# Performance work log

Measured on AMD Instinct MI355X. Metric: run time of the kernel, lower is better.

The kernel has to match this reference:

```python
import jax, jax.numpy as jnp
import numpy as np

B, S, N, F, H = 8, 12, 4096, 4, 64  # batch, seq_len, num_nodes, input_dim, hidden_dim


def setup_inputs() -> dict:
    key = jax.random.key(0)
    ks = jax.random.split(key, 16)
    sc = 0.05
    adj = jax.random.uniform(ks[0], (N, N), jnp.float32) * (2.0 / N)  # ~row-normalized Laplacian
    return {
        "X": jax.random.normal(ks[1], (B, S, N, F), jnp.float32),
        "adj": adj,
        "struc_emb": jax.random.normal(ks[2], (N, H), jnp.float32),
        "W1": jax.random.normal(ks[3], (H + F, 3 * H), jnp.float32) * sc,
        "b1": jnp.ones((3 * H,), jnp.float32),  # bias=1.0 init in graph_conv1
        "W2": jax.random.normal(ks[4], (H + F, H), jnp.float32) * sc,
        "b2": jnp.zeros((H,), jnp.float32),
        "W_ih": jax.random.normal(ks[5], (4 * H, H), jnp.float32) * sc,
        "W_hh": jax.random.normal(ks[6], (4 * H, H), jnp.float32) * sc,
        "b_ih": jnp.zeros((4 * H,), jnp.float32),
        "b_hh": jnp.zeros((4 * H,), jnp.float32),
        "D1": jax.random.normal(ks[7], (H, H // 2), jnp.float32) * sc,
        "bd1": jnp.zeros((H // 2,), jnp.float32),
        "D2": jax.random.normal(ks[8], (H // 2, 1), jnp.float32) * sc,
        "bd2": jnp.zeros((1,), jnp.float32),
    }


def _graph_conv(adj, x_t, h_flat, W, b, out_dim):
    # x_t: [B,N,F]; h_flat: [B, N*H]
    h = h_flat.reshape(B, N, H)
    cat = jnp.concatenate([x_t, h], axis=-1)            # [B,N,F+H]
    a = jnp.einsum('mn,bnf->bmf', adj, cat)             # laplacian diffusion
    out = a @ W + b                                     # [B,N,out_dim]
    return out.reshape(B, N * out_dim)


def reference(X, adj, struc_emb, W1, b1, W2, b2, W_ih, W_hh, b_ih, b_hh, D1, bd1, D2, bd2):
    # ---- encoder: TGTCCellLSTM unrolled over time (cell_state never updated, as in source) ----
    h0 = jnp.broadcast_to(struc_emb.reshape(1, N * H), (B, N * H))
    c0 = h0  # cell returns old cell_state, so it stays the struc_emb forever (faithful)

    def enc_step(h, x_t):
        g = jax.nn.sigmoid(_graph_conv(adj, x_t, h, W1, b1, 3 * H))   # [B, N*3H]
        f, i, o = jnp.split(g, 3, axis=1)                             # flat chunk, as in torch code
        conv = _graph_conv(adj, x_t, h, W2, b2, H)                    # [B, N*H]
        c = f * c0 + i * jnp.tanh(conv)
        h_new = o * jnp.tanh(c)
        return h_new, None

    h_last, _ = jax.lax.scan(enc_step, h0, jnp.swapaxes(X, 0, 1))  # scan over S
    z = h_last.reshape(B, N, H)

    # ---- decoder: 1-layer LSTM fed the same z at every step, then 2-layer MLP to scalar ----
    x_dec = z.reshape(B * N, H)
    x_gates = x_dec @ W_ih.T + b_ih + b_hh  # input contribution constant across steps

    def dec_step(carry, _):
        h, c = carry
        gates = x_gates + h @ W_hh.T
        i, f, g, o = jnp.split(gates, 4, axis=1)  # torch LSTM gate order
        c = jax.nn.sigmoid(f) * c + jax.nn.sigmoid(i) * jnp.tanh(g)
        h = jax.nn.sigmoid(o) * jnp.tanh(c)
        return (h, c), h

    zeros = jnp.zeros((B * N, H), X.dtype)
    _, hs = jax.lax.scan(dec_step, (zeros, zeros), None, length=S)  # [S, B*N, H]
    hs = jnp.swapaxes(hs, 0, 1)                                      # [B*N, S, H]
    d = jax.nn.relu(hs @ D1 + bd1) @ D2 + bd2                        # [B*N, S, 1]
    recon = d.reshape(B, S, N)  # flat reshape from (B*N, S), matching torch reshape semantics
    return (z, recon)
```

## Files before the change

kernel.cpp:

```cpp
#include <hip/hip_runtime.h>
#include <cstdint>
#include <cstddef>


typedef unsigned short u16;
typedef short s8v __attribute__((ext_vector_type(8)));
typedef unsigned short h8v __attribute__((ext_vector_type(8)));
typedef float f4v __attribute__((ext_vector_type(4)));
typedef int   i4v __attribute__((ext_vector_type(4)));

__device__ __forceinline__ u16 f2bf(float x){
  union { float f; uint32_t u; } v; v.f = x;
  uint32_t r = v.u + 0x7FFFu + ((v.u >> 16) & 1u);
  return (u16)(r >> 16);
}
__device__ __forceinline__ float bf2f(u16 x){
  union { uint32_t u; float f; } v; v.u = ((uint32_t)x) << 16; return v.f;
}
__device__ __forceinline__ float frcp(float x){ return __builtin_amdgcn_rcpf(x); }
__device__ __forceinline__ float fsig(float x){ return frcp(1.0f + __expf(-x)); }
__device__ __forceinline__ float ftanh(float x){ return 1.0f - 2.0f * frcp(1.0f + __expf(2.0f * x)); }
__device__ __forceinline__ int8_t f2i8(float x){
  int v = (int)rintf(x);
  v = v > 127 ? 127 : (v < -127 ? -127 : v);
  return (int8_t)v;
}

typedef const __attribute__((address_space(1))) unsigned int* gp_t;
typedef __attribute__((address_space(3))) unsigned int* lp_t;
__device__ __forceinline__ void glds16(const void* g, void* l){
  __builtin_amdgcn_global_load_lds((gp_t)g, (lp_t)l, 16, 0, 0);
}

__device__ __forceinline__ void s1_core(int8_t* As, int8_t* Bs,
    const int8_t* __restrict__ A, const int8_t* __restrict__ Bt,
    u16* __restrict__ Cs, int Ncols, int ksl, float cscale,
    int mb, int nb, int k0)
{
  const int t  = threadIdx.x;
  const int l  = t & 63;
  const int w  = t >> 6;
  const int wm = (w >> 1) * 64;
  const int wc = (w & 1) * 64;

  i4v acc[4][4];
  #pragma unroll
  for (int i = 0; i < 4; ++i)
    #pragma unroll
    for (int j = 0; j < 4; ++j) acc[i][j] = (i4v)0;

  const int srow = t >> 3;
  const int gsw  = ((t & 7) ^ (srow & 7)) * 16;
  const int8_t* ab = A  + (size_t)(mb + srow) * 4096 + k0 + gsw;
  const int8_t* bb = Bt + (size_t)(nb + srow) * 4096 + k0 + gsw;

  const int rA = l & 15;
  const int lsw = l & 7;

  #pragma unroll
  for (int j = 0; j < 4; ++j) {
    glds16(ab + (size_t)(32 * j) * 4096, As + j * 4096 + t * 16);
    glds16(bb + (size_t)(32 * j) * 4096, Bs + j * 4096 + t * 16);
  }

  for (int kk = 0; kk < ksl; kk += 128) {
    const int cur = (kk >> 7) & 1;
    __syncthreads();
    if (kk + 128 < ksl) {
      const int nxt = cur ^ 1;
      #pragma unroll
      for (int j = 0; j < 4; ++j) {
        glds16(ab + (size_t)(32 * j) * 4096 + kk + 128, As + nxt * 16384 + j * 4096 + t * 16);
        glds16(bb + (size_t)(32 * j) * 4096 + kk + 128, Bs + nxt * 16384 + j * 4096 + t * 16);
      }
    }
    const int bofs = cur * 16384;
    #pragma unroll
    for (int sub = 0; sub < 2; ++sub) {
      const int kpos = ((sub * 4 + (l >> 4)) ^ lsw) * 16;
      i4v af[4], bf[4];
      #pragma unroll
      for (int mt = 0; mt < 4; ++mt)
        af[mt] = *(const i4v*)&As[bofs + (wm + mt * 16 + rA) * 128 + kpos];
      #pragma unroll
      for (int nt = 0; nt < 4; ++nt)
        bf[nt] = *(const i4v*)&Bs[bofs + (wc + nt * 16 + rA) * 128 + kpos];
      #pragma unroll
      for (int mt = 0; mt < 4; ++mt)
        #pragma unroll
        for (int nt = 0; nt < 4; ++nt)
          acc[mt][nt] = __builtin_amdgcn_mfma_i32_16x16x64_i8(af[mt], bf[nt], acc[mt][nt], 0, 0, 0);
    }
  }

  const int colo = l & 15;
  const int rowo = (l >> 4) * 4;
  #pragma unroll
  for (int mt = 0; mt < 4; ++mt)
    #pragma unroll
    for (int nt = 0; nt < 4; ++nt)
      #pragma unroll
      for (int r = 0; r < 4; ++r) {
        int gr = mb + wm + mt * 16 + rowo + r;
        int gc = nb + wc + nt * 16 + colo;
        Cs[(size_t)gr * Ncols + gc] = f2bf((float)acc[mt][nt][r] * cscale);
      }
}

__global__ __launch_bounds__(256)
void gemm_s1_i8(const int8_t* __restrict__ A, const int8_t* __restrict__ Bt,
                u16* __restrict__ Cpart, int Ncols, int ksl, float cscale)
{
  __shared__ int8_t As[2 * 128 * 128];
  __shared__ int8_t Bs[2 * 128 * 128];
  s1_core(As, Bs, A, Bt, Cpart + (size_t)blockIdx.z * 4096 * Ncols,
          Ncols, ksl, cscale, blockIdx.x * 128, blockIdx.y * 128,
          blockIdx.z * ksl);
}

__global__ __launch_bounds__(256)
void gemm_s1_comb(const int8_t* __restrict__ A, const int8_t* __restrict__ Xp,
                  const int8_t* __restrict__ PB,
                  u16* __restrict__ CpX, u16* __restrict__ CpH,
                  int ksl, float cs)
{
  __shared__ int8_t As[2 * 128 * 128];
  __shared__ int8_t Bs[2 * 128 * 128];
  const int by = blockIdx.y;
  if (by < 3)
    s1_core(As, Bs, A, Xp, CpX + (size_t)blockIdx.z * 4096 * 384,
            384, ksl, cs, blockIdx.x * 128, by * 128, blockIdx.z * ksl);
  else
    s1_core(As, Bs, A, PB, CpH + (size_t)blockIdx.z * 4096 * 512,
            512, ksl, cs, blockIdx.x * 128, (by - 3) * 128, blockIdx.z * ksl);
}

__global__ __launch_bounds__(256)
void reduceN(const u16* __restrict__ P, u16* __restrict__ O, size_t SL)
{
  size_t i = ((size_t)blockIdx.x * 256 + threadIdx.x) * 8;
  if (i >= SL) return;
  float s[8] = {0,0,0,0,0,0,0,0};
  #pragma unroll
  for (int z = 0; z < 4; ++z) {
    uint4 v = *(const uint4*)(P + z * SL + i);
    uint32_t wd[4] = {v.x, v.y, v.z, v.w};
    #pragma unroll
    for (int q = 0; q < 4; ++q) {
      union { uint32_t u; float f; } lo, hi;
      lo.u = wd[q] << 16; hi.u = wd[q] & 0xFFFF0000u;
      s[2*q] += lo.f; s[2*q+1] += hi.f;
    }
  }
  uint4 o; uint32_t* ow = (uint32_t*)&o;
  #pragma unroll
  for (int q = 0; q < 4; ++q)
    ow[q] = (uint32_t)f2bf(s[2*q]) | ((uint32_t)f2bf(s[2*q+1]) << 16);
  *(uint4*)(O + i) = o;
}

__global__ __launch_bounds__(256)
void gemm_s2(const u16* __restrict__ AH, const u16* __restrict__ AXb,
             const u16* __restrict__ WTf, const float* __restrict__ b1v,
             const float* __restrict__ b2v, u16* __restrict__ G, int tstep)
{
  __shared__ u16 As[64 * 104];
  const int t = threadIdx.x;
  const int l = t & 63, w = t >> 6;
  const int wm = (w >> 1) * 32, wc0 = (w & 1) * 32;
  const int mb = blockIdx.x * 64;
  const size_t SL = 32768ull * 64;

  #pragma unroll
  for (int pass = 0; pass < 2; ++pass) {
    int idx = t + pass * 256;
    int row = idx >> 3, oct = idx & 7;
    size_t base = (size_t)(mb + row) * 64 + oct * 8;
    float s[8] = {0,0,0,0,0,0,0,0};
    #pragma unroll
    for (int z = 0; z < 4; ++z) {
      uint4 v = *(const uint4*)(AH + z * SL + base);
      uint32_t wd[4] = {v.x, v.y, v.z, v.w};
      #pragma unroll
      for (int q = 0; q < 4; ++q) {
        union { uint32_t u; float f; } lo, hi;
        lo.u = wd[q] << 16; hi.u = wd[q] & 0xFFFF0000u;
        s[2*q] += lo.f; s[2*q+1] += hi.f;
      }
    }
    uint4 o; uint32_t* ow = (uint32_t*)&o;
    #pragma unroll
    for (int q = 0; q < 4; ++q)
      ow[q] = (uint32_t)f2bf(s[2*q]) | ((uint32_t)f2bf(s[2*q+1]) << 16);
    *(uint4*)&As[row * 104 + oct * 8] = o;
  }
  {
    int row = t >> 2, q = t & 3;
    uint4 o = {0, 0, 0, 0};
    if (q == 0) {
      int r = mb + row, n = r >> 3, b = r & 7;
      const uint32_t* src = (const uint32_t*)(AXb + (size_t)n * 384 + tstep * 32 + b * 4);
      o.x = src[0]; o.y = src[1];
    }
    *(uint4*)&As[row * 104 + 64 + q * 8] = o;
  }
  __syncthreads();

  const int rA = l & 15, kg = (l >> 4) * 8;
  s8v af[3][2];
  #pragma unroll
  for (int kc = 0; kc < 3; ++kc)
    #pragma unroll
    for (int mt = 0; mt < 2; ++mt)
      af[kc][mt] = *(const s8v*)&As[(wm + mt * 16 + rA) * 104 + kc * 32 + kg];

  const int lchunk = ((l & 15) * 4 + (l >> 4)) * 8;
  const int colo = l & 15, rowo = (l >> 4) * 4;
  #pragma unroll
  for (int nb4 = 0; nb4 < 4; ++nb4) {
    const int wc = nb4 * 64 + wc0;
    f4v acc[2][2];
    #pragma unroll
    for (int i = 0; i < 2; ++i)
      #pragma unroll
      for (int j = 0; j < 2; ++j) acc[i][j] = (f4v)0.0f;
    #pragma unroll
    for (int kc = 0; kc < 3; ++kc) {
      s8v bf[2];
      #pragma unroll
      for (int nt = 0; nt < 2; ++nt) {
        int ct = nb4 * 4 + (w & 1) * 2 + nt;
        bf[nt] = *(const s8v*)&WTf[(ct * 3 + kc) * 512 + lchunk];
      }
      #pragma unroll
      for (int mt = 0; mt < 2; ++mt)
        #pragma unroll
        for (int nt = 0; nt < 2; ++nt)
          acc[mt][nt] = __builtin_amdgcn_mfma_f32_16x16x32_bf16(af[kc][mt], bf[nt], acc[mt][nt], 0, 0, 0);
    }
    #pragma unroll
    for (int mt = 0; mt < 2; ++mt)
      #pragma unroll
      for (int nt = 0; nt < 2; ++nt) {
        int gc = wc + nt * 16 + colo;
        float bb = (gc < 192) ? b1v[gc] : b2v[gc - 192];
        #pragma unroll
        for (int r = 0; r < 4; ++r) {
          int gr = mb + wm + mt * 16 + rowo + r;
          int np = gr >> 3, b = gr & 7;
          float v = acc[mt][nt][r] + bb;
          size_t addr;
          u16 val;
          if (gc < 192) {
            int p = np * 192 + gc;
            int role = p >> 18;
            int k = p & 262143;
            addr = ((size_t)(role * 8 + b) << 18) + k;
            val = f2bf(fsig(v));
          } else {
            int k = np * 64 + (gc - 192);
            addr = ((size_t)(24 + b) << 18) + k;
            val = f2bf(ftanh(v));
          }
          G[addr] = val;
        }
      }
  }
}

__global__ __launch_bounds__(256)
void enc_update(const u16* __restrict__ G, const float* __restrict__ struc,
                int8_t* __restrict__ PB)
{
  __shared__ uint8_t hx[64 * 40];
  const int t = threadIdx.x;
  const int b = blockIdx.x >> 7;
  const int n0 = (blockIdx.x & 127) * 32;
  const int k8 = n0 * 64 + t * 8;
  const int nloc = t >> 3;
  const int hh0 = (t & 7) * 8;

  h8v f8 = *(const h8v*)&G[((size_t)(     b) << 18) + k8];
  h8v i8_ = *(const h8v*)&G[((size_t)( 8 + b) << 18) + k8];
  h8v o8 = *(const h8v*)&G[((size_t)(16 + b) << 18) + k8];
  h8v c8 = *(const h8v*)&G[((size_t)(24 + b) << 18) + k8];
  float4 s0 = *(const float4*)&struc[k8];
  float4 s1 = *(const float4*)&struc[k8 + 4];
  float sv[8] = {s0.x, s0.y, s0.z, s0.w, s1.x, s1.y, s1.z, s1.w};

  #pragma unroll
  for (int j = 0; j < 8; ++j) {
    float c = bf2f(f8[j]) * sv[j] + bf2f(i8_[j]) * bf2f(c8[j]);
    float hv = bf2f(o8[j]) * ftanh(c);
    hx[(hh0 + j) * 40 + nloc] = (uint8_t)f2i8(hv * 127.0f);
  }
  __syncthreads();
  {
    int row = t >> 2, seg = t & 3;
    uint2 v = *(const uint2*)&hx[row * 40 + seg * 8];
    *(uint2*)&PB[(size_t)(b * 64 + row) * 4096 + n0 + seg * 8] = v;
  }
}

__global__ __launch_bounds__(256)
void setup_all(const float* __restrict__ adj, int8_t* __restrict__ adj_i8,
               const float* __restrict__ W1, const float* __restrict__ W2,
               const float* __restrict__ Wih, const float* __restrict__ Whh,
               const float* __restrict__ D1,
               u16* __restrict__ WTf, u16* __restrict__ WihB,
               u16* __restrict__ WhhB, u16* __restrict__ D1t,
               const float* __restrict__ struc, int8_t* __restrict__ PB,
               const float* __restrict__ X, int8_t* __restrict__ Xp)
{
  const int blk = blockIdx.x;
  const int t = threadIdx.x;
  if (blk < 16384) {
    size_t i = ((size_t)blk * 256 + t) * 4;
    float4 v = *(const float4*)(adj + i);
    const float s = 127.0f * 2048.0f;
    char4 o;
    o.x = f2i8(v.x * s); o.y = f2i8(v.y * s); o.z = f2i8(v.z * s); o.w = f2i8(v.w * s);
    *(char4*)(adj_i8 + i) = o;
  } else if (blk < 16616) {
    int gid = (blk - 16384) * 256 + t;
    if (gid < 24576) {
      int f = gid >> 9;
      int q = gid & 511;
      int ct = f / 3, kc = f - ct * 3;
      int c = q >> 3, e = q & 7;
      int rA = c >> 2, g = c & 3;
      int row = ct * 16 + rA;
      int ch = kc * 32 + g * 8 + e;
      float v = 0.0f;
      int rr = (ch < 64) ? (ch + 4) : (ch < 68 ? ch - 64 : -1);
      if (rr >= 0) v = (row < 192) ? W1[(size_t)rr * 192 + row] : W2[(size_t)rr * 64 + (row - 192)];
      WTf[gid] = f2bf(v);
    } else if (gid < 40960) {
      int q = gid - 24576; WihB[q] = f2bf(Wih[q]);
    } else if (gid < 57344) {
      int q = gid - 40960; WhhB[q] = f2bf(Whh[q]);
    } else if (gid < 59392) {
      int q = gid - 57344;
      int j = q >> 6, hh = q & 63;
      D1t[q] = f2bf(D1[(size_t)hh * 32 + j]);
    }
  } else if (blk < 24808) {
    int gid = (blk - 16616) * 256 + t;
    int n = gid & 4095;
    int r = gid >> 12;
    int hh = r & 63;
    PB[(size_t)r * 4096 + n] = f2i8(struc[(size_t)n * 64 + hh] * 25.4f);
  } else {
    int gid = (blk - 24808) * 256 + t;
    int n = gid & 4095;
    int col = gid >> 12;
    int ts = col >> 5, r = col & 31, b = r >> 2, f = r & 3;
    Xp[(size_t)col * 4096 + n] = f2i8(X[(((size_t)(b * 12 + ts)) * 4096 + n) * 4 + f] * 25.4f);
  }
}

#define DSTR 80
__global__ __launch_bounds__(512, 4)
void dec_fused(const u16* __restrict__ G, const float* __restrict__ struc,
               float* __restrict__ zout,
               const u16* __restrict__ WihB, const u16* __restrict__ WhhB,
               const float* __restrict__ bih, const float* __restrict__ bhh,
               const u16* __restrict__ D1t, const float* __restrict__ bd1,
               const float* __restrict__ D2, const float* __restrict__ bd2,
               float* __restrict__ recon)
{
  __shared__ u16 whl[256 * DSTR];
  __shared__ u16 hl[64 * DSTR];
  __shared__ u16 zl[64 * DSTR];
  const int t = threadIdx.x;
  const int l = t & 63;
  const int w = t >> 6;
  const int wg = w >> 1;
  const int half = w & 1;
  const int r0 = blockIdx.x * 64;
  const int rA = l & 15;
  const int kg = (l >> 4) * 8;

  for (int c = t; c < 2048; c += 512) {
    int j = c >> 3, k8 = (c & 7) * 8;
    *(uint4*)&whl[j * DSTR + k8] = *(const uint4*)&WhhB[j * 64 + k8];
  }

  {
    const int b = r0 >> 12;
    const size_t base = (size_t)(r0 & 4095) * 64 + t * 8;
    h8v f8 = *(const h8v*)&G[((size_t)(     b) << 18) + base];
    h8v i8_ = *(const h8v*)&G[((size_t)( 8 + b) << 18) + base];
    h8v o8 = *(const h8v*)&G[((size_t)(16 + b) << 18) + base];
    h8v c8 = *(const h8v*)&G[((size_t)(24 + b) << 18) + base];
    float4 s0 = *(const float4*)&struc[base];
    float4 s1 = *(const float4*)&struc[base + 4];
    float sv[8] = {s0.x, s0.y, s0.z, s0.w, s1.x, s1.y, s1.z, s1.w};
    float hv[8];
    #pragma unroll
    for (int j = 0; j < 8; ++j) {
      float c = bf2f(f8[j]) * sv[j] + bf2f(i8_[j]) * bf2f(c8[j]);
      hv[j] = bf2f(o8[j]) * ftanh(c);
    }
    float4 z0 = {hv[0], hv[1], hv[2], hv[3]};
    float4 z1 = {hv[4], hv[5], hv[6], hv[7]};
    *(float4*)&zout[((size_t)b << 18) + base] = z0;
    *(float4*)&zout[((size_t)b << 18) + base + 4] = z1;
    h8v zb;
    #pragma unroll
    for (int j = 0; j < 8; ++j) zb[j] = f2bf(hv[j]);
    *(h8v*)&zl[(t >> 3) * DSTR + (t & 7) * 8] = zb;
  }
  __syncthreads();

  f4v xg[8];
  {
    s8v a0 = *(const s8v*)&zl[(wg * 16 + rA) * DSTR + kg];
    s8v a1 = *(const s8v*)&zl[(wg * 16 + rA) * DSTR + 32 + kg];
    #pragma unroll
    for (int j = 0; j < 8; ++j) {
      int nt = (j >> 1) * 4 + half * 2 + (j & 1);
      s8v b0 = *(const s8v*)&WihB[(nt * 16 + rA) * 64 + kg];
      s8v b1 = *(const s8v*)&WihB[(nt * 16 + rA) * 64 + 32 + kg];
      f4v a = (f4v)0.0f;
      a = __builtin_amdgcn_mfma_f32_16x16x32_bf16(a0, b0, a, 0, 0, 0);
      a = __builtin_amdgcn_mfma_f32_16x16x32_bf16(a1, b1, a, 0, 0, 0);
      float bb = bih[nt * 16 + rA] + bhh[nt * 16 + rA];
      #pragma unroll
      for (int r = 0; r < 4; ++r) xg[j][r] = a[r] + bb;
    }
  }
  s8v d1f[4];
  #pragma unroll
  for (int nt2 = 0; nt2 < 2; ++nt2)
    #pragma unroll
    for (int kc = 0; kc < 2; ++kc)
      d1f[nt2 * 2 + kc] = *(const s8v*)&D1t[(nt2 * 16 + rA) * 64 + kc * 32 + kg];
  const float bd1x = bd1[rA], bd1y = bd1[16 + rA];
  const float d2x = D2[rA], d2y = D2[16 + rA];
  const float bd2v = bd2[0];

  float cst[8];
  #pragma unroll
  for (int q = 0; q < 8; ++q) cst[q] = 0.0f;
  s8v ha0 = (s8v)0, ha1 = (s8v)0;

  for (int s = 0; s < 12; ++s) {
    f4v acc[8];
    #pragma unroll
    for (int j = 0; j < 8; ++j) acc[j] = xg[j];
    if (s > 0) {
      #pragma unroll
      for (int j = 0; j < 8; ++j) {
        int nt = (j >> 1) * 4 + half * 2 + (j & 1);
        s8v b0 = *(const s8v*)&whl[(nt * 16 + rA) * DSTR + kg];
        s8v b1 = *(const s8v*)&whl[(nt * 16 + rA) * DSTR + 32 + kg];
        acc[j] = __builtin_amdgcn_mfma_f32_16x16x32_bf16(ha0, b0, acc[j], 0, 0, 0);
        acc[j] = __builtin_amdgcn_mfma_f32_16x16x32_bf16(ha1, b1, acc[j], 0, 0, 0);
      }
    }
    __syncthreads();
    #pragma unroll
    for (int ql = 0; ql < 2; ++ql) {
      int q = half * 2 + ql;
      #pragma unroll
      for (int r = 0; r < 4; ++r) {
        float i_ = fsig (acc[0 + ql][r]);
        float f_ = fsig (acc[2 + ql][r]);
        float g_ = ftanh(acc[4 + ql][r]);
        float o_ = fsig (acc[6 + ql][r]);
        float cc = f_ * cst[ql * 4 + r] + i_ * g_;
        cst[ql * 4 + r] = cc;
        float hv = o_ * ftanh(cc);
        hl[(wg * 16 + (l >> 4) * 4 + r) * DSTR + q * 16 + rA] = f2bf(hv);
      }
    }
    __syncthreads();
    ha0 = *(const s8v*)&hl[(wg * 16 + rA) * DSTR + kg];
    ha1 = *(const s8v*)&hl[(wg * 16 + rA) * DSTR + 32 + kg];
    if (half == 0) {
      f4v m0 = (f4v)0.0f, m1 = (f4v)0.0f;
      m0 = __builtin_amdgcn_mfma_f32_16x16x32_bf16(ha0, d1f[0], m0, 0, 0, 0);
      m0 = __builtin_amdgcn_mfma_f32_16x16x32_bf16(ha1, d1f[1], m0, 0, 0, 0);
      m1 = __builtin_amdgcn_mfma_f32_16x16x32_bf16(ha0, d1f[2], m1, 0, 0, 0);
      m1 = __builtin_amdgcn_mfma_f32_16x16x32_bf16(ha1, d1f[3], m1, 0, 0, 0);
      f4v p;
      #pragma unroll
      for (int r = 0; r < 4; ++r)
        p[r] = fmaxf(m0[r] + bd1x, 0.0f) * d2x + fmaxf(m1[r] + bd1y, 0.0f) * d2y;
      #pragma unroll
      for (int mask = 1; mask < 16; mask <<= 1)
        #pragma unroll
        for (int r = 0; r < 4; ++r) p[r] += __shfl_xor(p[r], mask);
      if (rA < 4)
        recon[(size_t)(r0 + wg * 16 + (l >> 4) * 4 + rA) * 12 + s] = p[rA] + bd2v;
    }
  }
}

extern "C" void kernel_launch(void* const* d_in, const int* in_sizes, int n_in,
                              void* d_out, int out_size, void* d_ws, size_t ws_size,
                              hipStream_t stream)
{
  (void)in_sizes; (void)n_in; (void)out_size; (void)ws_size;
  const float* X     = (const float*)d_in[0];
  const float* adj   = (const float*)d_in[1];
  const float* struc = (const float*)d_in[2];
  const float* W1    = (const float*)d_in[3];
  const float* b1    = (const float*)d_in[4];
  const float* W2    = (const float*)d_in[5];
  const float* b2    = (const float*)d_in[6];
  const float* Wih   = (const float*)d_in[7];
  const float* Whh   = (const float*)d_in[8];
  const float* bih   = (const float*)d_in[9];
  const float* bhh   = (const float*)d_in[10];
  const float* D1    = (const float*)d_in[11];
  const float* bd1   = (const float*)d_in[12];
  const float* D2    = (const float*)d_in[13];
  const float* bd2   = (const float*)d_in[14];

  char* ws = (char*)d_ws;
  size_t off = 0;
  auto alloc = [&](size_t bytes){ void* p = ws + off; off += (bytes + 255) & ~(size_t)255; return p; };
  int8_t* adj_i8 = (int8_t*)alloc(4096ull * 4096);
  int8_t* PB     = (int8_t*)alloc(512ull * 4096);
  int8_t* Xp     = (int8_t*)alloc(384ull * 4096);
  u16*   AXb    = (u16*)  alloc(4096ull * 384 * 2);
  u16*   Cpart  = (u16*)  alloc(4ull * 4096 * 512 * 2);
  u16*   CpartX = (u16*)  alloc(4ull * 4096 * 384 * 2);
  u16*   G      = (u16*)  alloc(4ull * 8 * 262144 * 2);
  u16*   WTf    = (u16*)  alloc(256ull * 96 * 2);
  u16*   WihB   = (u16*)  alloc(256ull * 64 * 2);
  u16*   WhhB   = (u16*)  alloc(256ull * 64 * 2);
  u16*   D1t    = (u16*)  alloc(32ull * 64 * 2);

  float* zout  = (float*)d_out;
  float* recon = (float*)d_out + 2097152;

  const float cs5 = (float)(2.0 / 4096.0 * 5.0 / (127.0 * 127.0));
  const float cs1 = (float)(2.0 / 4096.0 * 1.0 / (127.0 * 127.0));

  setup_all<<<30952, 256, 0, stream>>>(adj, adj_i8, W1, W2, Wih, Whh, D1,
                                       WTf, WihB, WhhB, D1t, struc, PB, X, Xp);
  gemm_s1_comb<<<dim3(32, 7, 4), 256, 0, stream>>>(adj_i8, Xp, PB, CpartX, Cpart,
                                                   1024, cs5);
  reduceN<<<768, 256, 0, stream>>>(CpartX, AXb, 4096ull * 384);

  for (int t = 0; t < 12; ++t) {
    if (t > 0)
      gemm_s1_i8<<<dim3(32, 4, 4), 256, 0, stream>>>(adj_i8, PB, Cpart, 512, 1024, cs1);
    gemm_s2<<<512, 256, 0, stream>>>(Cpart, AXb, WTf, b1, b2, G, t);
    if (t < 11)
      enc_update<<<1024, 256, 0, stream>>>(G, struc, PB);
  }

  dec_fused<<<512, 512, 0, stream>>>(G, struc, zout, WihB, WhhB, bih, bhh,
                                     D1t, bd1, D2, bd2, recon);
}
```

Before: 549.1 us.

## Enlarge int8 GEMM tile to 256x128 with 512-thread blocks

```diff
diff --git a/kernel.cpp b/kernel.cpp
--- a/kernel.cpp
+++ b/kernel.cpp
@@ -58,10 +58,11 @@
   const int lsw = l & 7;
 
   #pragma unroll
-  for (int j = 0; j < 4; ++j) {
-    glds16(ab + (size_t)(32 * j) * 4096, As + j * 4096 + t * 16);
-    glds16(bb + (size_t)(32 * j) * 4096, Bs + j * 4096 + t * 16);
-  }
+  for (int j = 0; j < 4; ++j)
+    glds16(ab + (size_t)(64 * j) * 4096, As + j * 8192 + t * 16);
+  #pragma unroll
+  for (int j = 0; j < 2; ++j)
+    glds16(bb + (size_t)(64 * j) * 4096, Bs + j * 8192 + t * 16);
 
   for (int kk = 0; kk < ksl; kk += 128) {
     const int cur = (kk >> 7) & 1;
@@ -69,11 +70,13 @@
     if (kk + 128 < ksl) {
       const int nxt = cur ^ 1;
       #pragma unroll
-      for (int j = 0; j < 4; ++j) {
-        glds16(ab + (size_t)(32 * j) * 4096 + kk + 128, As + nxt * 16384 + j * 4096 + t * 16);
-        glds16(bb + (size_t)(32 * j) * 4096 + kk + 128, Bs + nxt * 16384 + j * 4096 + t * 16);
-      }
-    }
+      for (int j = 0; j < 4; ++j)
+        glds16(ab + (size_t)(64 * j) * 4096 + kk + 128, As + nxt * 32768 + j * 8192 + t * 16);
+      #pragma unroll
+      for (int j = 0; j < 2; ++j)
+        glds16(bb + (size_t)(64 * j) * 4096 + kk + 128, Bs + nxt * 16384 + j * 8192 + t * 16);
+    }
+    const int aofs = cur * 32768;
     const int bofs = cur * 16384;
     #pragma unroll
     for (int sub = 0; sub < 2; ++sub) {
@@ -81,7 +84,7 @@
       i4v af[4], bf[4];
       #pragma unroll
       for (int mt = 0; mt < 4; ++mt)
-        af[mt] = *(const i4v*)&As[bofs + (wm + mt * 16 + rA) * 128 + kpos];
+        af[mt] = *(const i4v*)&As[aofs + (wm + mt * 16 + rA) * 128 + kpos];
       #pragma unroll
       for (int nt = 0; nt < 4; ++nt)
         bf[nt] = *(const i4v*)&Bs[bofs + (wc + nt * 16 + rA) * 128 + kpos];
@@ -107,32 +110,35 @@
       }
 }
 
-__global__ __launch_bounds__(256)
+__global__ __launch_bounds__(512)
 void gemm_s1_i8(const int8_t* __restrict__ A, const int8_t* __restrict__ Bt,
                 u16* __restrict__ Cpart, int Ncols, int ksl, float cscale)
 {
-  __shared__ int8_t As[2 * 128 * 128];
-  __shared__ int8_t Bs[2 * 128 * 128];
-  s1_core(As, Bs, A, Bt, Cpart + (size_t)blockIdx.z * 4096 * Ncols,
-          Ncols, ksl, cscale, blockIdx.x * 128, blockIdx.y * 128,
+  __shared__ __align__(16) int8_t lds[98304];
+  s1_core(lds, lds + 65536, A, Bt, Cpart + (size_t)blockIdx.z * 4096 * Ncols,
+          Ncols, ksl, cscale, blockIdx.x * 256, blockIdx.y * 128,
           blockIdx.z * ksl);
 }
 
-__global__ __launch_bounds__(256)
+__global__ __launch_bounds__(512)
 void gemm_s1_comb(const int8_t* __restrict__ A, const int8_t* __restrict__ Xp,
                   const int8_t* __restrict__ PB,
                   u16* __restrict__ CpX, u16* __restrict__ CpH,
                   int ksl, float cs)
 {
-  __shared__ int8_t As[2 * 128 * 128];
-  __shared__ int8_t Bs[2 * 128 * 128];
-  const int by = blockIdx.y;
-  if (by < 3)
-    s1_core(As, Bs, A, Xp, CpX + (size_t)blockIdx.z * 4096 * 384,
-            384, ksl, cs, blockIdx.x * 128, by * 128, blockIdx.z * ksl);
-  else
-    s1_core(As, Bs, A, PB, CpH + (size_t)blockIdx.z * 4096 * 512,
-            512, ksl, cs, blockIdx.x * 128, (by - 3) * 128, blockIdx.z * ksl);
+  __shared__ __align__(16) int8_t lds[98304];
+  const int bid = blockIdx.x;
+  if (bid < 256) {
+    const int bx = bid & 15, by = (bid >> 4) & 3, bz = bid >> 6;
+    s1_core(lds, lds + 65536, A, PB, CpH + (size_t)bz * 4096 * 512,
+            512, ksl, cs, bx * 256, by * 128, bz * ksl);
+  } else {
+    const int q = bid - 256;
+    const int bx = q & 15, s = q >> 4;
+    const int by = s % 3, bz = s / 3;
+    s1_core(lds, lds + 65536, A, Xp, CpX + (size_t)bz * 4096 * 384,
+            384, ksl, cs, bx * 256, by * 128, bz * ksl);
+  }
 }
 
 __global__ __launch_bounds__(256)
@@ -542,13 +548,12 @@
 
   setup_all<<<30952, 256, 0, stream>>>(adj, adj_i8, W1, W2, Wih, Whh, D1,
                                        WTf, WihB, WhhB, D1t, struc, PB, X, Xp);
-  gemm_s1_comb<<<dim3(32, 7, 4), 256, 0, stream>>>(adj_i8, Xp, PB, CpartX, Cpart,
-                                                   1024, cs5);
+  gemm_s1_comb<<<448, 512, 0, stream>>>(adj_i8, Xp, PB, CpartX, Cpart, 1024, cs5);
   reduceN<<<768, 256, 0, stream>>>(CpartX, AXb, 4096ull * 384);
 
   for (int t = 0; t < 12; ++t) {
     if (t > 0)
-      gemm_s1_i8<<<dim3(32, 4, 4), 256, 0, stream>>>(adj_i8, PB, Cpart, 512, 1024, cs1);
+      gemm_s1_i8<<<dim3(16, 4, 4), 512, 0, stream>>>(adj_i8, PB, Cpart, 512, 1024, cs1);
     gemm_s2<<<512, 256, 0, stream>>>(Cpart, AXb, WTf, b1, b2, G, t);
     if (t < 11)
       enc_update<<<1024, 256, 0, stream>>>(G, struc, PB);
```

Result: no change. 559.8 us (+2.0%).
